# Kernel optimization log

Hardware: AMD Instinct MI355X
Metric: run time of the kernel (lower is better)

## Reference

```python
import jax, jax.numpy as jnp
import numpy as np

B, P, E, C = 64, 10000, 128, 100


def setup_inputs() -> dict:
    key = jax.random.key(0)
    k1, k2, k3, k4 = jax.random.split(key, 4)
    encoded_nodes = jax.random.normal(k1, (B, P, E), dtype=jnp.float32)
    cluster_ids = jax.random.randint(k2, (B, P), 0, C, dtype=jnp.int64)
    # nn.Linear(E, E) params
    lim = 1.0 / np.sqrt(E)
    proj_w = jax.random.uniform(k3, (E, E), dtype=jnp.float32, minval=-lim, maxval=lim)
    proj_b = jax.random.uniform(k4, (E,), dtype=jnp.float32, minval=-lim, maxval=lim)
    return {"encoded_nodes": encoded_nodes, "cluster_ids": cluster_ids,
            "num_clusters": C, "proj_w": proj_w, "proj_b": proj_b}


def reference(encoded_nodes, cluster_ids, num_clusters, proj_w, proj_b):
    ids = cluster_ids.astype(jnp.int32)  # [B, P]

    def seg_sum(x, i):
        return jax.ops.segment_sum(x, i, num_segments=num_clusters)

    # per-batch scatter-add of node embeddings and counts
    sums = jax.vmap(seg_sum)(encoded_nodes, ids)                     # [B, C, E]
    ones = jnp.ones(encoded_nodes.shape[:2], encoded_nodes.dtype)    # [B, P]
    counts = jax.vmap(seg_sum)(ones, ids)[..., None]                  # [B, C, 1]

    cluster_embs = sums / jnp.maximum(counts, 1.0)                    # mean pooling
    cluster_embs = cluster_embs @ proj_w.T + proj_b                   # Linear(E, E)

    # gather each node's (projected) cluster embedding back
    idx = jnp.broadcast_to(ids[:, :, None], encoded_nodes.shape)      # [B, P, E]
    g_node = jnp.take_along_axis(cluster_embs, idx, axis=1)           # [B, P, E]
    return cluster_embs, g_node
```

## Files before the change

### kernel.cpp

```cpp
#include <hip/hip_runtime.h>

#define BB 64
#define PP 10000
#define EE 128
#define CC 100

#define ESL 4
#define SLICE 32
#define NP 8
#define CHUNK (PP / NP)
#define PSUM_STRIDE (CC * SLICE)
#define PSUM_NPSTRIDE (BB * ESL * PSUM_STRIDE)

__global__ __launch_bounds__(256) void scatter_kernel(
    const float* __restrict__ nodes, const int* __restrict__ ids,
    float* __restrict__ psums, float* __restrict__ pcnts)
{
    __shared__ float s_acc[CC * SLICE];
    __shared__ float s_cnt[CC];
    __shared__ int   s_ids[CHUNK];

    const int tid = threadIdx.x;
    const int es  = blockIdx.x;
    const int b   = blockIdx.y;
    const int np  = blockIdx.z;

    for (int i = tid; i < CC * SLICE; i += 256) s_acc[i] = 0.f;
    if (tid < CC) s_cnt[tid] = 0.f;

    const int p0 = np * CHUNK;
    const int* idb = ids + b * PP + p0;
    for (int i = tid; i < CHUNK; i += 256) s_ids[i] = idb[i];
    __syncthreads();

    const int lane = tid & 31;
    const int sub  = tid >> 5;
    const float* src = nodes + (size_t)b * PP * EE + (size_t)p0 * EE
                             + es * SLICE + lane;

    if (es == 0) {
#pragma unroll 4
        for (int p = sub; p < CHUNK; p += 8) {
            int c = s_ids[p];
            float v = src[(size_t)p * EE];
            if ((unsigned)c < CC) {
                atomicAdd(&s_acc[c * SLICE + lane], v);
                if (lane == 0) atomicAdd(&s_cnt[c], 1.0f);
            }
        }
    } else {
#pragma unroll 4
        for (int p = sub; p < CHUNK; p += 8) {
            int c = s_ids[p];
            float v = src[(size_t)p * EE];
            if ((unsigned)c < CC) atomicAdd(&s_acc[c * SLICE + lane], v);
        }
    }
    __syncthreads();

    float* out = psums + (size_t)((np * BB + b) * ESL + es) * PSUM_STRIDE;
    for (int i = tid; i < CC * SLICE; i += 256) out[i] = s_acc[i];
    if (es == 0) {
        float* oc = pcnts + (np * BB + b) * CC;
        for (int i = tid; i < CC; i += 256) oc[i] = s_cnt[i];
    }
}

__global__ __launch_bounds__(256) void project_kernel(
    float* __restrict__ ce,
    const float* __restrict__ psums,
    const float* __restrict__ pcnts,
    const float* __restrict__ W,
    const float* __restrict__ bias)
{
    __shared__ float s_wt[EE * 129];
    __shared__ float s_mt[EE * 8];
    __shared__ float s_inv[8];

    const int tid = threadIdx.x;
    for (int i = tid; i < EE * EE; i += 256) {
        int e = i >> 7, k = i & 127;
        s_wt[k * 129 + e] = W[i];
    }

    const int e   = tid & 127;
    const int sub = tid >> 7;
    const float be = bias[e];
    const int row0 = blockIdx.x * 16;

    for (int j = 0; j < 2; ++j) {
        __syncthreads();
        if (tid < 8) {
            int row = row0 + j * 8 + tid;
            float s = 0.f;
#pragma unroll
            for (int np = 0; np < NP; ++np) s += pcnts[np * (BB * CC) + row];
            s_inv[tid] = 1.0f / fmaxf(s, 1.0f);
        }
        for (int i = tid; i < 8 * EE; i += 256) {
            int ee = i & 127, rr = i >> 7;
            int row = row0 + j * 8 + rr;
            int bb = row / CC, c = row % CC;
            const float* pp = psums + (size_t)(bb * ESL + (ee >> 5)) * PSUM_STRIDE
                                    + c * SLICE + (ee & 31);
            float s = 0.f;
#pragma unroll
            for (int np = 0; np < NP; ++np) s += pp[(size_t)np * PSUM_NPSTRIDE];
            s_mt[ee * 8 + rr] = s;
        }
        __syncthreads();

        float acc0 = 0.f, acc1 = 0.f, acc2 = 0.f, acc3 = 0.f;
        const float* wp = &s_wt[e];
        const float4* mp = (const float4*)s_mt;
#pragma unroll 8
        for (int k = 0; k < 128; ++k) {
            float  w = wp[k * 129];
            float4 m = mp[k * 2 + sub];
            acc0 = fmaf(w, m.x, acc0);
            acc1 = fmaf(w, m.y, acc1);
            acc2 = fmaf(w, m.z, acc2);
            acc3 = fmaf(w, m.w, acc3);
        }
        const int rbase = row0 + j * 8 + sub * 4;
        ce[(size_t)(rbase + 0) * EE + e] = be + acc0 * s_inv[sub * 4 + 0];
        ce[(size_t)(rbase + 1) * EE + e] = be + acc1 * s_inv[sub * 4 + 1];
        ce[(size_t)(rbase + 2) * EE + e] = be + acc2 * s_inv[sub * 4 + 2];
        ce[(size_t)(rbase + 3) * EE + e] = be + acc3 * s_inv[sub * 4 + 3];
    }
}

__global__ __launch_bounds__(256) void gather_kernel(
    const int* __restrict__ ids, const float* __restrict__ ce,
    float* __restrict__ gn)
{
    const int tid  = threadIdx.x;
    const int lane = tid & 31;
    const int sub  = tid >> 5;
    const int b    = blockIdx.y;

    const int* idb = ids + b * PP;
    const float4* ceb = (const float4*)(ce + (size_t)b * CC * EE);
    float4* dst = (float4*)(gn + (size_t)b * PP * EE);

    for (int p = blockIdx.x * 8 + sub; p < PP; p += 32 * 8) {
        int c = idb[p];
        if ((unsigned)c >= CC) c = 0;
        float4 v = ceb[(size_t)c * 32 + lane];
        dst[(size_t)p * 32 + lane] = v;
    }
}

extern "C" void kernel_launch(void* const* d_in, const int* in_sizes, int n_in,
                              void* d_out, int out_size, void* d_ws, size_t ws_size,
                              hipStream_t stream)
{
    const float* nodes = (const float*)d_in[0];
    const int*   ids   = (const int*)d_in[1];
    const float* W     = (const float*)d_in[3];
    const float* bias  = (const float*)d_in[4];

    float* out = (float*)d_out;
    float* ce  = out;
    float* gn  = out + (size_t)BB * CC * EE;

    float* psums = gn;
    float* pcnts = gn + (size_t)NP * PSUM_NPSTRIDE;

    hipLaunchKernelGGL(scatter_kernel, dim3(ESL, BB, NP), dim3(256), 0, stream,
                       nodes, ids, psums, pcnts);
    hipLaunchKernelGGL(project_kernel, dim3(BB * CC / 16), dim3(256), 0, stream,
                       ce, psums, pcnts, W, bias);
    hipLaunchKernelGGL(gather_kernel, dim3(32, BB), dim3(256), 0, stream,
                       ids, ce, gn);
}
```

Baseline: 934.4 us.

## Scatter full embedding rows with float4 loads and plane-interleaved LDS accumulators

Drops the four-way embedding-slice split in the scatter kernel. Each block now handles a whole 128-wide row using float4 loads and accumulates into a 100x128 LDS buffer laid out as four planes, doubling the number of point chunks to 16. The project kernel reduces 16 partials and remaps the plane-interleaved layout back to embedding order, and partial and output stores become nontemporal. The aim is fewer redundant id reads and wider global loads, at the cost of 51KB of LDS per block (limiting occupancy) and twice as many partials to reduce.

```diff
diff --git a/kernel.cpp b/kernel.cpp
--- a/kernel.cpp
+++ b/kernel.cpp
@@ -4,28 +4,26 @@
 #define PP 10000
 #define EE 128
 #define CC 100
+#define NP 16
+#define CHUNK (PP / NP)
+#define ROWS (CC * EE)
+#define PLANE (CC * 32)
 
-#define ESL 4
-#define SLICE 32
-#define NP 8
-#define CHUNK (PP / NP)
-#define PSUM_STRIDE (CC * SLICE)
-#define PSUM_NPSTRIDE (BB * ESL * PSUM_STRIDE)
+typedef float v4f __attribute__((ext_vector_type(4)));
 
 __global__ __launch_bounds__(256) void scatter_kernel(
     const float* __restrict__ nodes, const int* __restrict__ ids,
     float* __restrict__ psums, float* __restrict__ pcnts)
 {
-    __shared__ float s_acc[CC * SLICE];
+    __shared__ float s_acc[ROWS];
     __shared__ float s_cnt[CC];
     __shared__ int   s_ids[CHUNK];
 
     const int tid = threadIdx.x;
-    const int es  = blockIdx.x;
-    const int b   = blockIdx.y;
-    const int np  = blockIdx.z;
+    const int b   = blockIdx.x;
+    const int np  = blockIdx.y;
 
-    for (int i = tid; i < CC * SLICE; i += 256) s_acc[i] = 0.f;
+    for (int i = tid; i < ROWS; i += 256) s_acc[i] = 0.f;
     if (tid < CC) s_cnt[tid] = 0.f;
 
     const int p0 = np * CHUNK;
@@ -35,35 +33,31 @@
 
     const int lane = tid & 31;
     const int sub  = tid >> 5;
-    const float* src = nodes + (size_t)b * PP * EE + (size_t)p0 * EE
-                             + es * SLICE + lane;
+    const v4f* src = (const v4f*)(nodes + (size_t)b * PP * EE
+                                        + (size_t)p0 * EE);
 
-    if (es == 0) {
 #pragma unroll 4
-        for (int p = sub; p < CHUNK; p += 8) {
-            int c = s_ids[p];
-            float v = src[(size_t)p * EE];
-            if ((unsigned)c < CC) {
-                atomicAdd(&s_acc[c * SLICE + lane], v);
-                if (lane == 0) atomicAdd(&s_cnt[c], 1.0f);
-            }
-        }
-    } else {
-#pragma unroll 4
-        for (int p = sub; p < CHUNK; p += 8) {
-            int c = s_ids[p];
-            float v = src[(size_t)p * EE];
-            if ((unsigned)c < CC) atomicAdd(&s_acc[c * SLICE + lane], v);
+    for (int p = sub; p < CHUNK; p += 8) {
+        int c = s_ids[p];
+        v4f v = src[(size_t)p * 32 + lane];
+        if ((unsigned)c < CC) {
+            float* a = &s_acc[c * 32 + lane];
+            __hip_atomic_fetch_add(a + 0 * PLANE, v.x, __ATOMIC_RELAXED, __HIP_MEMORY_SCOPE_WORKGROUP);
+            __hip_atomic_fetch_add(a + 1 * PLANE, v.y, __ATOMIC_RELAXED, __HIP_MEMORY_SCOPE_WORKGROUP);
+            __hip_atomic_fetch_add(a + 2 * PLANE, v.z, __ATOMIC_RELAXED, __HIP_MEMORY_SCOPE_WORKGROUP);
+            __hip_atomic_fetch_add(a + 3 * PLANE, v.w, __ATOMIC_RELAXED, __HIP_MEMORY_SCOPE_WORKGROUP);
+            if (lane == 0)
+                __hip_atomic_fetch_add(&s_cnt[c], 1.0f, __ATOMIC_RELAXED, __HIP_MEMORY_SCOPE_WORKGROUP);
         }
     }
     __syncthreads();
 
-    float* out = psums + (size_t)((np * BB + b) * ESL + es) * PSUM_STRIDE;
-    for (int i = tid; i < CC * SLICE; i += 256) out[i] = s_acc[i];
-    if (es == 0) {
-        float* oc = pcnts + (np * BB + b) * CC;
-        for (int i = tid; i < CC; i += 256) oc[i] = s_cnt[i];
-    }
+    v4f* outp = (v4f*)(psums + (size_t)(np * BB + b) * ROWS);
+    const v4f* accp = (const v4f*)s_acc;
+    for (int i = tid; i < ROWS / 4; i += 256)
+        __builtin_nontemporal_store(accp[i], &outp[i]);
+    float* oc = pcnts + (np * BB + b) * CC;
+    if (tid < CC) __builtin_nontemporal_store(s_cnt[tid], &oc[tid]);
 }
 
 __global__ __launch_bounds__(256) void project_kernel(
@@ -94,29 +88,32 @@
             int row = row0 + j * 8 + tid;
             float s = 0.f;
 #pragma unroll
-            for (int np = 0; np < NP; ++np) s += pcnts[np * (BB * CC) + row];
+            for (int np = 0; np < NP; ++np)
+                s += pcnts[np * (BB * CC) + row];
             s_inv[tid] = 1.0f / fmaxf(s, 1.0f);
         }
         for (int i = tid; i < 8 * EE; i += 256) {
-            int ee = i & 127, rr = i >> 7;
+            int rr = i >> 7, idx = i & 127;
             int row = row0 + j * 8 + rr;
             int bb = row / CC, c = row % CC;
-            const float* pp = psums + (size_t)(bb * ESL + (ee >> 5)) * PSUM_STRIDE
-                                    + c * SLICE + (ee & 31);
+            const float* pp = psums + (size_t)bb * ROWS
+                                    + (idx >> 5) * PLANE + c * 32 + (idx & 31);
             float s = 0.f;
 #pragma unroll
-            for (int np = 0; np < NP; ++np) s += pp[(size_t)np * PSUM_NPSTRIDE];
+            for (int np = 0; np < NP; ++np)
+                s += __builtin_nontemporal_load(pp + (size_t)np * BB * ROWS);
+            int ee = ((idx & 31) << 2) | (idx >> 5);
             s_mt[ee * 8 + rr] = s;
         }
         __syncthreads();
 
         float acc0 = 0.f, acc1 = 0.f, acc2 = 0.f, acc3 = 0.f;
         const float* wp = &s_wt[e];
-        const float4* mp = (const float4*)s_mt;
+        const v4f* mp = (const v4f*)s_mt;
 #pragma unroll 8
         for (int k = 0; k < 128; ++k) {
-            float  w = wp[k * 129];
-            float4 m = mp[k * 2 + sub];
+            float w = wp[k * 129];
+            v4f   m = mp[k * 2 + sub];
             acc0 = fmaf(w, m.x, acc0);
             acc1 = fmaf(w, m.y, acc1);
             acc2 = fmaf(w, m.z, acc2);
@@ -140,14 +137,15 @@
     const int b    = blockIdx.y;
 
     const int* idb = ids + b * PP;
-    const float4* ceb = (const float4*)(ce + (size_t)b * CC * EE);
-    float4* dst = (float4*)(gn + (size_t)b * PP * EE);
+    const v4f* ceb = (const v4f*)(ce + (size_t)b * CC * EE);
+    v4f* dst = (v4f*)(gn + (size_t)b * PP * EE);
 
+#pragma unroll 2
     for (int p = blockIdx.x * 8 + sub; p < PP; p += 32 * 8) {
         int c = idb[p];
         if ((unsigned)c >= CC) c = 0;
-        float4 v = ceb[(size_t)c * 32 + lane];
-        dst[(size_t)p * 32 + lane] = v;
+        v4f v = ceb[(size_t)c * 32 + lane];
+        __builtin_nontemporal_store(v, &dst[(size_t)p * 32 + lane]);
     }
 }
 
@@ -165,9 +163,9 @@
     float* gn  = out + (size_t)BB * CC * EE;
 
     float* psums = gn;
-    float* pcnts = gn + (size_t)NP * PSUM_NPSTRIDE;
+    float* pcnts = gn + (size_t)NP * BB * ROWS;
 
-    hipLaunchKernelGGL(scatter_kernel, dim3(ESL, BB, NP), dim3(256), 0, stream,
+    hipLaunchKernelGGL(scatter_kernel, dim3(BB, NP), dim3(256), 0, stream,
                        nodes, ids, psums, pcnts);
     hipLaunchKernelGGL(project_kernel, dim3(BB * CC / 16), dim3(256), 0, stream,
                        ce, psums, pcnts, W, bias);
```

Result: faster. 886.7 us (-5.1%).
